# Optimization experiments

Hardware: AMD Instinct MI355X
Metric: run time of the kernel (lower is better)

Reference implementation:

```python
import jax, jax.numpy as jnp
import numpy as np

LAMB = 4.0
TH = -4.0 / LAMB  # threshold from APELoss.__init__
LOSS_WEIGHT = 1.0


def setup_inputs() -> dict:
    key = jax.random.key(0)
    k1, k2 = jax.random.split(key)
    N = 151552  # total anchors
    F = 1024    # foreground anchors (placed first so masks have static shape)
    logits = jax.random.normal(k1, (N,), dtype=jnp.float32)
    targets = jnp.concatenate([jnp.ones((F,), jnp.int32), jnp.zeros((N - F,), jnp.int32)])
    ious = jax.random.uniform(k2, (F,), dtype=jnp.float32)
    return {"logits": logits, "targets": targets, "ious": ious, "num_fg": F}


def reference(logits, targets, ious, num_fg):
    # targets is constructed with all fg (==1) in the first num_fg slots,
    # so logits[targets==1] == logits[:num_fg] (static-shape equivalent).
    fg = logits[:num_fg]          # [F] foreground logits
    bg = logits[num_fg:]          # [B] background logits (targets==0)
    p_min = jnp.min(fg)
    rel_bg = bg >= p_min + TH     # relevant background selection

    # Pairwise fg-vs-bg: [F, B]
    diff_bg = (bg[None, :] - fg[:, None]) * LAMB
    neg_mask = rel_bg[None, :] & (bg[None, :] > fg[:, None] + TH)

    # Pairwise fg-vs-fg: [F, F]
    diff_fg = (fg[None, :] - fg[:, None]) * LAMB
    above = fg[None, :] > fg[:, None] + TH
    pos_mask = (ious[None, :] < ious[:, None]) & above   # lower-IoU fg act as negatives
    tp_mask = (ious[None, :] >= ious[:, None]) & above   # higher/equal-IoU fg are TPs

    # rank = sum sigmoid(FP) + sum sigmoid(TP)  (detached in original)
    fp_sum = (jnp.sum(jax.nn.sigmoid(diff_bg) * neg_mask, axis=1)
              + jnp.sum(jax.nn.sigmoid(diff_fg) * pos_mask, axis=1))
    tp_sum = jnp.sum(jax.nn.sigmoid(diff_fg) * tp_mask, axis=1)
    rank = jax.lax.stop_gradient(fp_sum + tp_sum)

    # BCE(sigmoid(z), 0) = -log(1 - sigmoid(z)) = softplus(z)  (stable form)
    dist = (jnp.sum(jax.nn.softplus(diff_bg) * neg_mask, axis=1)
            + jnp.sum(jax.nn.softplus(diff_fg) * pos_mask, axis=1))

    # Original only appends a loss term when FP_dis is non-empty.
    count = jnp.sum(neg_mask, axis=1) + jnp.sum(pos_mask, axis=1)
    valid = count > 0
    safe_rank = jnp.where(valid, rank, 1.0)
    per = jnp.where(valid, dist * ious / safe_rank, 0.0)
    n_valid = jnp.maximum(jnp.sum(valid), 1)

    return LOSS_WEIGHT * jnp.sum(per) / n_valid.astype(per.dtype) / LAMB
```

## Files before the change

kernel.cpp:

```cpp
#include <hip/hip_runtime.h>
#include <hip/hip_bf16.h>


#define APE_LAMB 4.0f
#define APE_KC   5.770780163555856f
#define APE_LN2  0.6931471805599453f
#define NINF     (-__builtin_inff())

__device__ __forceinline__ float exp2g(float x) { return __builtin_amdgcn_exp2f(x); }
__device__ __forceinline__ float log2g(float x) { return __builtin_amdgcn_logf(x); }
__device__ __forceinline__ float rcpg(float x)  { return __builtin_amdgcn_rcpf(x); }

constexpr int   B_BINS  = 1024;
constexpr int   NB      = 8;
constexpr int   TPB     = 256;
constexpr float BIN_LO  = -5.12f;
constexpr float BIN_DL  = 0.01f;
constexpr float BIN_INV = 100.0f;
constexpr float M1SCALE = 268435456.0f;
constexpr float M1INV   = 3.725290298461914e-09f;
constexpr int   ROWS_E  = 4;
constexpr int   ROWS_B  = 4;

#define ST_AGENT(p, v) __hip_atomic_store((p), (v), __ATOMIC_RELAXED, __HIP_MEMORY_SCOPE_AGENT)
#define LD_AGENT(p)    __hip_atomic_load((p), __ATOMIC_RELAXED, __HIP_MEMORY_SCOPE_AGENT)

__global__ __launch_bounds__(TPB) void ape_phase1(
    const float* __restrict__ logits, const float* __restrict__ ious,
    int F, int M, int chunkH,
    float* __restrict__ gC, float* __restrict__ gM, float* __restrict__ bmaxA,
    float* __restrict__ dist2, float* __restrict__ rank2, float* __restrict__ cnt2,
    int* __restrict__ ctr)
{
    const int tid  = threadIdx.x;
    const int lane = tid & 63, wid = tid >> 6;

    if (blockIdx.x == 0 && tid == 0) *ctr = 0;

    if ((int)blockIdx.x < NB) {
        __shared__ int hc[B_BINS];
        __shared__ int hm[B_BINS];
        for (int b = tid; b < B_BINS; b += TPB) { hc[b] = 0; hm[b] = 0; }
        __syncthreads();

        const float* bg = logits + F;
        const int start = (int)blockIdx.x * chunkH;
        const int end   = min(start + chunkH, M);
        float bmax = NINF;

        for (int j = start + tid * 4; j < end; j += TPB * 4) {
            float v[4];
            if (j + 4 <= end) {
                float4 q = *reinterpret_cast<const float4*>(bg + j);
                v[0] = q.x; v[1] = q.y; v[2] = q.z; v[3] = q.w;
            } else {
#pragma unroll
                for (int k = 0; k < 4; ++k) v[k] = (j + k < end) ? bg[j + k] : NINF;
            }
#pragma unroll
            for (int k = 0; k < 4; ++k) {
                if (j + k >= end) continue;
                float x = v[k];
                bmax = fmaxf(bmax, x);
                int b = (int)((x - BIN_LO) * BIN_INV);
                b = min(max(b, 0), B_BINS - 1);
                float c = fmaf((float)b, BIN_DL, BIN_LO + 0.5f * BIN_DL);
                int q = __float2int_rn((x - c) * M1SCALE);
                atomicAdd(&hc[b], 1);
                atomicAdd(&hm[b], q);
            }
        }
        __syncthreads();
        const int base = (int)blockIdx.x * B_BINS;
        for (int b = tid; b < B_BINS; b += TPB) {
            gC[base + b] = (float)hc[b];
            gM[base + b] = (float)hm[b] * M1INV;
        }
        __shared__ float rm[4];
        for (int off = 32; off > 0; off >>= 1) bmax = fmaxf(bmax, __shfl_down(bmax, off));
        if (lane == 0) rm[wid] = bmax;
        __syncthreads();
        if (tid == 0)
            bmaxA[blockIdx.x] = fmaxf(fmaxf(rm[0], rm[1]), fmaxf(rm[2], rm[3]));
    } else {
        const int i0 = ((int)blockIdx.x - NB) * ROWS_B;
        float fgl[ROWS_B], ioui[ROWS_B];
#pragma unroll
        for (int r = 0; r < ROWS_B; ++r) {
            int i = i0 + r;
            fgl[r]  = (i < F) ? logits[i] * APE_KC : __builtin_inff();
            ioui[r] = (i < F) ? ious[i] : 0.f;
        }
        float dist[ROWS_B], rank[ROWS_B], cnt[ROWS_B];
#pragma unroll
        for (int r = 0; r < ROWS_B; ++r) { dist[r]=0.f; rank[r]=0.f; cnt[r]=0.f; }

        for (int j = tid; j < F; j += TPB) {
            float fjl  = logits[j] * APE_KC;
            float iouj = ious[j];
#pragma unroll
            for (int r = 0; r < ROWS_B; ++r) {
                float dl = fjl - fgl[r];
                bool above = dl > -APE_KC;
                float dm = above ? dl : NINF;
                float u  = exp2g(dm);
                float o  = 1.0f + u;
                float sig = 1.0f - rcpg(o);
                float spl = log2g(o);
                bool pos = iouj < ioui[r];
                rank[r] += sig;
                dist[r] += pos ? spl : 0.f;
                cnt[r]  += (above && pos) ? 1.f : 0.f;
            }
        }
        __shared__ float redf[4][ROWS_B * 3];
#pragma unroll
        for (int r = 0; r < ROWS_B; ++r) {
            float d = dist[r], a = rank[r], c = cnt[r];
            for (int off = 32; off > 0; off >>= 1) {
                d += __shfl_down(d, off);
                a += __shfl_down(a, off);
                c += __shfl_down(c, off);
            }
            if (lane == 0) { redf[wid][r*3+0]=d; redf[wid][r*3+1]=a; redf[wid][r*3+2]=c; }
        }
        __syncthreads();
        if (tid < ROWS_B * 3) {
            float sum = redf[0][tid] + redf[1][tid] + redf[2][tid] + redf[3][tid];
            int r = tid / 3, q = tid % 3;
            int i = i0 + r;
            if (i < F) {
                if      (q == 0) dist2[i] = sum;
                else if (q == 1) rank2[i] = sum;
                else             cnt2[i]  = sum;
            }
        }
    }
}

__global__ __launch_bounds__(TPB) void ape_phase2(
    const float* __restrict__ logits, const float* __restrict__ ious, int F, int EB,
    const float* __restrict__ gC, const float* __restrict__ gM,
    const float* __restrict__ bmaxA,
    const float* __restrict__ dist2, const float* __restrict__ rank2,
    const float* __restrict__ cnt2,
    float* __restrict__ pp, float* __restrict__ pv,
    int* __restrict__ ctr, float* __restrict__ out)
{
    const int tid  = threadIdx.x;
    const int lane = tid & 63, wid = tid >> 6;

    __shared__ float2 h[B_BINS];
    for (int b = tid; b < B_BINS; b += TPB) {
        float c = 0.f, m = 0.f;
#pragma unroll
        for (int s = 0; s < NB; ++s) {
            c += gC[s * B_BINS + b];
            m += gM[s * B_BINS + b];
        }
        h[b] = make_float2(c, m);
    }

    const int i0 = (int)blockIdx.x * ROWS_E;
    float fKC[ROWS_E];
#pragma unroll
    for (int r = 0; r < ROWS_E; ++r) {
        int i = i0 + r;
        fKC[r] = (i < F) ? logits[i] * APE_KC : __builtin_inff();
    }
    __syncthreads();

    float rk[ROWS_E], dt[ROWS_E];
#pragma unroll
    for (int r = 0; r < ROWS_E; ++r) { rk[r] = 0.f; dt[r] = 0.f; }

    for (int it = 0; it < B_BINS; it += TPB) {
        const int b = it + tid;
        float2 cm = h[b];
        float cKC  = fmaf((float)b, BIN_DL * APE_KC, (BIN_LO + 0.5f * BIN_DL) * APE_KC);
        float m1x4 = cm.y * APE_LAMB;
        float m1kc = cm.y * APE_KC;
#pragma unroll
        for (int r = 0; r < ROWS_E; ++r) {
            float dl = cKC - fKC[r];
            float dm = (dl > -APE_KC) ? dl : NINF;
            float u  = exp2g(dm);
            float o  = 1.0f + u;
            float rr = rcpg(o);
            float lg = log2g(o);
            float s  = 1.0f - rr;
            rk[r] = fmaf(cm.x, s,  rk[r]);
            rk[r] = fmaf(m1x4, s * rr, rk[r]);
            dt[r] = fmaf(cm.x, lg, dt[r]);
            dt[r] = fmaf(m1kc, s,  dt[r]);
        }
    }

    __shared__ float red[4][ROWS_E * 2];
#pragma unroll
    for (int r = 0; r < ROWS_E; ++r) {
        float a = rk[r], d = dt[r];
        for (int off = 32; off > 0; off >>= 1) {
            a += __shfl_down(a, off);
            d += __shfl_down(d, off);
        }
        if (lane == 0) { red[wid][r*2+0] = a; red[wid][r*2+1] = d; }
    }
    __syncthreads();

    __shared__ int lastFlag;
    if (tid == 0) {
        float gmax = NINF;
#pragma unroll
        for (int k = 0; k < NB; ++k) gmax = fmaxf(gmax, bmaxA[k]);
        float sper = 0.f, sval = 0.f;
#pragma unroll
        for (int r = 0; r < ROWS_E; ++r) {
            int i = i0 + r;
            if (i < F) {
                float rowRank = red[0][r*2+0] + red[1][r*2+0] + red[2][r*2+0] + red[3][r*2+0];
                float rowDist = red[0][r*2+1] + red[1][r*2+1] + red[2][r*2+1] + red[3][r*2+1];
                float rkv = rowRank + rank2[i];
                float dtv = (rowDist + dist2[i]) * APE_LN2;
                bool valid = (gmax > logits[i] - 1.0f) || (cnt2[i] > 0.f);
                if (valid) {
                    sper += dtv * ious[i] / rkv;
                    sval += 1.f;
                }
            }
        }
        ST_AGENT(&pp[blockIdx.x], sper);
        ST_AGENT(&pv[blockIdx.x], sval);
        asm volatile("s_waitcnt vmcnt(0)" ::: "memory");
        int old = __hip_atomic_fetch_add(ctr, 1, __ATOMIC_RELAXED,
                                         __HIP_MEMORY_SCOPE_AGENT);
        lastFlag = (old == EB - 1) ? 1 : 0;
    }
    __syncthreads();
    if (!lastFlag) return;

    float sp = 0.f, sv = 0.f;
    for (int k = tid; k < EB; k += TPB) {
        sp += LD_AGENT(&pp[k]);
        sv += LD_AGENT(&pv[k]);
    }
    __shared__ float rp[4], rv[4];
    for (int off = 32; off > 0; off >>= 1) {
        sp += __shfl_down(sp, off);
        sv += __shfl_down(sv, off);
    }
    if (lane == 0) { rp[wid] = sp; rv[wid] = sv; }
    __syncthreads();
    if (tid == 0) {
        float p = rp[0] + rp[1] + rp[2] + rp[3];
        float v = rv[0] + rv[1] + rv[2] + rv[3];
        out[0] = p / fmaxf(v, 1.f) / APE_LAMB;
    }
}

extern "C" void kernel_launch(void* const* d_in, const int* in_sizes, int n_in,
                              void* d_out, int out_size, void* d_ws, size_t ws_size,
                              hipStream_t stream) {
    const float* logits = (const float*)d_in[0];
    const float* ious   = (const float*)d_in[2];
    const int N = in_sizes[0];
    const int F = in_sizes[2];
    const int M = N - F;

    const int FB = (F + ROWS_B - 1) / ROWS_B;
    const int EB = (F + ROWS_E - 1) / ROWS_E;

    float* ws    = (float*)d_ws;
    float* gC    = ws;
    float* gM    = gC + NB * B_BINS;
    float* bmaxA = gM + NB * B_BINS;
    float* dist2 = bmaxA + NB;
    float* rank2 = dist2 + F;
    float* cnt2  = rank2 + F;
    float* pp    = cnt2 + F;
    float* pv    = pp + EB;
    int*   ctr   = (int*)(pv + EB);

    int chunkH = ((M + NB - 1) / NB + 3) & ~3;
    if (chunkH < 4) chunkH = 4;

    ape_phase1<<<NB + FB, TPB, 0, stream>>>(logits, ious, F, M, chunkH,
                                            gC, gM, bmaxA, dist2, rank2, cnt2, ctr);
    ape_phase2<<<EB, TPB, 0, stream>>>(logits, ious, F, EB, gC, gM, bmaxA,
                                       dist2, rank2, cnt2, pp, pv, ctr,
                                       (float*)d_out);
}
```

Before: 23.88 us.

## Fuse histogram and evaluation phases into one kernel with spin-wait on counter

Merges the two kernels into a single launch. Eight histogram blocks publish their partial bins and signal an atomic counter, and each evaluation block computes its fg-vs-fg sums before spin-waiting on that counter and then consuming the histogram. This removes one kernel launch and the global round-trip for per-row fg partials. It adds a memset launch and relies on the histogram blocks being scheduled while evaluator blocks spin, which is a deadlock risk if residency is insufficient. The 264 total blocks should fit on the device.

```diff
diff --git a/kernel.cpp b/kernel.cpp
--- a/kernel.cpp
+++ b/kernel.cpp
@@ -19,23 +19,20 @@
 constexpr float BIN_INV = 100.0f;
 constexpr float M1SCALE = 268435456.0f;
 constexpr float M1INV   = 3.725290298461914e-09f;
-constexpr int   ROWS_E  = 4;
-constexpr int   ROWS_B  = 4;
+constexpr int   ROWS    = 4;
 
 #define ST_AGENT(p, v) __hip_atomic_store((p), (v), __ATOMIC_RELAXED, __HIP_MEMORY_SCOPE_AGENT)
 #define LD_AGENT(p)    __hip_atomic_load((p), __ATOMIC_RELAXED, __HIP_MEMORY_SCOPE_AGENT)
 
-__global__ __launch_bounds__(TPB) void ape_phase1(
+__global__ __launch_bounds__(TPB) void ape_fused(
     const float* __restrict__ logits, const float* __restrict__ ious,
-    int F, int M, int chunkH,
+    int F, int M, int chunkH, int NEVAL,
     float* __restrict__ gC, float* __restrict__ gM, float* __restrict__ bmaxA,
-    float* __restrict__ dist2, float* __restrict__ rank2, float* __restrict__ cnt2,
-    int* __restrict__ ctr)
+    float* __restrict__ pp, float* __restrict__ pv,
+    int* __restrict__ ctr, float* __restrict__ out)
 {
     const int tid  = threadIdx.x;
     const int lane = tid & 63, wid = tid >> 6;
-
-    if (blockIdx.x == 0 && tid == 0) *ctr = 0;
 
     if ((int)blockIdx.x < NB) {
         __shared__ int hc[B_BINS];
@@ -73,106 +70,93 @@
         __syncthreads();
         const int base = (int)blockIdx.x * B_BINS;
         for (int b = tid; b < B_BINS; b += TPB) {
-            gC[base + b] = (float)hc[b];
-            gM[base + b] = (float)hm[b] * M1INV;
+            ST_AGENT(&gC[base + b], (float)hc[b]);
+            ST_AGENT(&gM[base + b], (float)hm[b] * M1INV);
         }
         __shared__ float rm[4];
         for (int off = 32; off > 0; off >>= 1) bmax = fmaxf(bmax, __shfl_down(bmax, off));
         if (lane == 0) rm[wid] = bmax;
         __syncthreads();
         if (tid == 0)
-            bmaxA[blockIdx.x] = fmaxf(fmaxf(rm[0], rm[1]), fmaxf(rm[2], rm[3]));
-    } else {
-        const int i0 = ((int)blockIdx.x - NB) * ROWS_B;
-        float fgl[ROWS_B], ioui[ROWS_B];
-#pragma unroll
-        for (int r = 0; r < ROWS_B; ++r) {
-            int i = i0 + r;
-            fgl[r]  = (i < F) ? logits[i] * APE_KC : __builtin_inff();
-            ioui[r] = (i < F) ? ious[i] : 0.f;
-        }
-        float dist[ROWS_B], rank[ROWS_B], cnt[ROWS_B];
-#pragma unroll
-        for (int r = 0; r < ROWS_B; ++r) { dist[r]=0.f; rank[r]=0.f; cnt[r]=0.f; }
-
-        for (int j = tid; j < F; j += TPB) {
-            float fjl  = logits[j] * APE_KC;
-            float iouj = ious[j];
-#pragma unroll
-            for (int r = 0; r < ROWS_B; ++r) {
-                float dl = fjl - fgl[r];
-                bool above = dl > -APE_KC;
-                float dm = above ? dl : NINF;
-                float u  = exp2g(dm);
-                float o  = 1.0f + u;
-                float sig = 1.0f - rcpg(o);
-                float spl = log2g(o);
-                bool pos = iouj < ioui[r];
-                rank[r] += sig;
-                dist[r] += pos ? spl : 0.f;
-                cnt[r]  += (above && pos) ? 1.f : 0.f;
-            }
-        }
-        __shared__ float redf[4][ROWS_B * 3];
-#pragma unroll
-        for (int r = 0; r < ROWS_B; ++r) {
-            float d = dist[r], a = rank[r], c = cnt[r];
-            for (int off = 32; off > 0; off >>= 1) {
-                d += __shfl_down(d, off);
-                a += __shfl_down(a, off);
-                c += __shfl_down(c, off);
-            }
-            if (lane == 0) { redf[wid][r*3+0]=d; redf[wid][r*3+1]=a; redf[wid][r*3+2]=c; }
-        }
-        __syncthreads();
-        if (tid < ROWS_B * 3) {
-            float sum = redf[0][tid] + redf[1][tid] + redf[2][tid] + redf[3][tid];
-            int r = tid / 3, q = tid % 3;
-            int i = i0 + r;
-            if (i < F) {
-                if      (q == 0) dist2[i] = sum;
-                else if (q == 1) rank2[i] = sum;
-                else             cnt2[i]  = sum;
-            }
-        }
-    }
-}
-
-__global__ __launch_bounds__(TPB) void ape_phase2(
-    const float* __restrict__ logits, const float* __restrict__ ious, int F, int EB,
-    const float* __restrict__ gC, const float* __restrict__ gM,
-    const float* __restrict__ bmaxA,
-    const float* __restrict__ dist2, const float* __restrict__ rank2,
-    const float* __restrict__ cnt2,
-    float* __restrict__ pp, float* __restrict__ pv,
-    int* __restrict__ ctr, float* __restrict__ out)
-{
-    const int tid  = threadIdx.x;
-    const int lane = tid & 63, wid = tid >> 6;
+            ST_AGENT(&bmaxA[blockIdx.x],
+                     fmaxf(fmaxf(rm[0], rm[1]), fmaxf(rm[2], rm[3])));
+        asm volatile("s_waitcnt vmcnt(0)" ::: "memory");
+        __syncthreads();
+        if (tid == 0)
+            __hip_atomic_fetch_add(&ctr[0], 1, __ATOMIC_RELAXED,
+                                   __HIP_MEMORY_SCOPE_AGENT);
+        return;
+    }
+
+    const int e  = (int)blockIdx.x - NB;
+    const int i0 = e * ROWS;
+
+    float fKC[ROWS], ioui[ROWS];
+#pragma unroll
+    for (int r = 0; r < ROWS; ++r) {
+        int i = i0 + r;
+        fKC[r]  = (i < F) ? logits[i] * APE_KC : __builtin_inff();
+        ioui[r] = (i < F) ? ious[i] : 0.f;
+    }
+
+    float fdist[ROWS], frank[ROWS], fcnt[ROWS];
+#pragma unroll
+    for (int r = 0; r < ROWS; ++r) { fdist[r]=0.f; frank[r]=0.f; fcnt[r]=0.f; }
+
+    for (int j = tid; j < F; j += TPB) {
+        float fjl  = logits[j] * APE_KC;
+        float iouj = ious[j];
+#pragma unroll
+        for (int r = 0; r < ROWS; ++r) {
+            float dl = fjl - fKC[r];
+            bool above = dl > -APE_KC;
+            float dm = above ? dl : NINF;
+            float u  = exp2g(dm);
+            float o  = 1.0f + u;
+            float sig = 1.0f - rcpg(o);
+            float spl = log2g(o);
+            bool pos = iouj < ioui[r];
+            frank[r] += sig;
+            fdist[r] += pos ? spl : 0.f;
+            fcnt[r]  += (above && pos) ? 1.f : 0.f;
+        }
+    }
+    __shared__ float redf[4][ROWS * 3];
+    __shared__ float fg3[ROWS * 3];
+#pragma unroll
+    for (int r = 0; r < ROWS; ++r) {
+        float a = frank[r], d = fdist[r], c = fcnt[r];
+        for (int off = 32; off > 0; off >>= 1) {
+            a += __shfl_down(a, off);
+            d += __shfl_down(d, off);
+            c += __shfl_down(c, off);
+        }
+        if (lane == 0) { redf[wid][r*3+0]=a; redf[wid][r*3+1]=d; redf[wid][r*3+2]=c; }
+    }
+    __syncthreads();
+    if (tid < ROWS * 3)
+        fg3[tid] = redf[0][tid] + redf[1][tid] + redf[2][tid] + redf[3][tid];
+
+    if (tid == 0) {
+        while (LD_AGENT(&ctr[0]) < NB) __builtin_amdgcn_s_sleep(8);
+    }
+    __syncthreads();
 
     __shared__ float2 h[B_BINS];
     for (int b = tid; b < B_BINS; b += TPB) {
         float c = 0.f, m = 0.f;
 #pragma unroll
         for (int s = 0; s < NB; ++s) {
-            c += gC[s * B_BINS + b];
-            m += gM[s * B_BINS + b];
+            c += LD_AGENT(&gC[s * B_BINS + b]);
+            m += LD_AGENT(&gM[s * B_BINS + b]);
         }
         h[b] = make_float2(c, m);
     }
-
-    const int i0 = (int)blockIdx.x * ROWS_E;
-    float fKC[ROWS_E];
-#pragma unroll
-    for (int r = 0; r < ROWS_E; ++r) {
-        int i = i0 + r;
-        fKC[r] = (i < F) ? logits[i] * APE_KC : __builtin_inff();
-    }
-    __syncthreads();
-
-    float rk[ROWS_E], dt[ROWS_E];
-#pragma unroll
-    for (int r = 0; r < ROWS_E; ++r) { rk[r] = 0.f; dt[r] = 0.f; }
+    __syncthreads();
+
+    float rk[ROWS], dt[ROWS];
+#pragma unroll
+    for (int r = 0; r < ROWS; ++r) { rk[r] = 0.f; dt[r] = 0.f; }
 
     for (int it = 0; it < B_BINS; it += TPB) {
         const int b = it + tid;
@@ -181,7 +165,7 @@
         float m1x4 = cm.y * APE_LAMB;
         float m1kc = cm.y * APE_KC;
 #pragma unroll
-        for (int r = 0; r < ROWS_E; ++r) {
+        for (int r = 0; r < ROWS; ++r) {
             float dl = cKC - fKC[r];
             float dm = (dl > -APE_KC) ? dl : NINF;
             float u  = exp2g(dm);
@@ -196,9 +180,9 @@
         }
     }
 
-    __shared__ float red[4][ROWS_E * 2];
-#pragma unroll
-    for (int r = 0; r < ROWS_E; ++r) {
+    __shared__ float red[4][ROWS * 2];
+#pragma unroll
+    for (int r = 0; r < ROWS; ++r) {
         float a = rk[r], d = dt[r];
         for (int off = 32; off > 0; off >>= 1) {
             a += __shfl_down(a, off);
@@ -212,35 +196,35 @@
     if (tid == 0) {
         float gmax = NINF;
 #pragma unroll
-        for (int k = 0; k < NB; ++k) gmax = fmaxf(gmax, bmaxA[k]);
+        for (int k = 0; k < NB; ++k) gmax = fmaxf(gmax, LD_AGENT(&bmaxA[k]));
         float sper = 0.f, sval = 0.f;
 #pragma unroll
-        for (int r = 0; r < ROWS_E; ++r) {
+        for (int r = 0; r < ROWS; ++r) {
             int i = i0 + r;
             if (i < F) {
                 float rowRank = red[0][r*2+0] + red[1][r*2+0] + red[2][r*2+0] + red[3][r*2+0];
                 float rowDist = red[0][r*2+1] + red[1][r*2+1] + red[2][r*2+1] + red[3][r*2+1];
-                float rkv = rowRank + rank2[i];
-                float dtv = (rowDist + dist2[i]) * APE_LN2;
-                bool valid = (gmax > logits[i] - 1.0f) || (cnt2[i] > 0.f);
+                float rkv = rowRank + fg3[r*3+0];
+                float dtv = (rowDist + fg3[r*3+1]) * APE_LN2;
+                bool valid = (gmax > logits[i] - 1.0f) || (fg3[r*3+2] > 0.f);
                 if (valid) {
                     sper += dtv * ious[i] / rkv;
                     sval += 1.f;
                 }
             }
         }
-        ST_AGENT(&pp[blockIdx.x], sper);
-        ST_AGENT(&pv[blockIdx.x], sval);
+        ST_AGENT(&pp[e], sper);
+        ST_AGENT(&pv[e], sval);
         asm volatile("s_waitcnt vmcnt(0)" ::: "memory");
-        int old = __hip_atomic_fetch_add(ctr, 1, __ATOMIC_RELAXED,
+        int old = __hip_atomic_fetch_add(&ctr[1], 1, __ATOMIC_RELAXED,
                                          __HIP_MEMORY_SCOPE_AGENT);
-        lastFlag = (old == EB - 1) ? 1 : 0;
+        lastFlag = (old == NEVAL - 1) ? 1 : 0;
     }
     __syncthreads();
     if (!lastFlag) return;
 
     float sp = 0.f, sv = 0.f;
-    for (int k = tid; k < EB; k += TPB) {
+    for (int k = tid; k < NEVAL; k += TPB) {
         sp += LD_AGENT(&pp[k]);
         sv += LD_AGENT(&pv[k]);
     }
@@ -254,7 +238,7 @@
     if (tid == 0) {
         float p = rp[0] + rp[1] + rp[2] + rp[3];
         float v = rv[0] + rv[1] + rv[2] + rv[3];
-        out[0] = p / fmaxf(v, 1.f) / APE_LAMB;
+        ST_AGENT(&out[0], p / fmaxf(v, 1.f) / APE_LAMB);
     }
 }
 
@@ -267,26 +251,21 @@
     const int F = in_sizes[2];
     const int M = N - F;
 
-    const int FB = (F + ROWS_B - 1) / ROWS_B;
-    const int EB = (F + ROWS_E - 1) / ROWS_E;
+    const int NEVAL = (F + ROWS - 1) / ROWS;
 
     float* ws    = (float*)d_ws;
     float* gC    = ws;
     float* gM    = gC + NB * B_BINS;
     float* bmaxA = gM + NB * B_BINS;
-    float* dist2 = bmaxA + NB;
-    float* rank2 = dist2 + F;
-    float* cnt2  = rank2 + F;
-    float* pp    = cnt2 + F;
-    float* pv    = pp + EB;
-    int*   ctr   = (int*)(pv + EB);
+    float* pp    = bmaxA + NB;
+    float* pv    = pp + NEVAL;
+    int*   ctr   = (int*)(pv + NEVAL);
 
     int chunkH = ((M + NB - 1) / NB + 3) & ~3;
     if (chunkH < 4) chunkH = 4;
 
-    ape_phase1<<<NB + FB, TPB, 0, stream>>>(logits, ious, F, M, chunkH,
-                                            gC, gM, bmaxA, dist2, rank2, cnt2, ctr);
-    ape_phase2<<<EB, TPB, 0, stream>>>(logits, ious, F, EB, gC, gM, bmaxA,
-                                       dist2, rank2, cnt2, pp, pv, ctr,
-                                       (float*)d_out);
+    hipMemsetAsync(ctr, 0, 2 * sizeof(int), stream);
+    ape_fused<<<NB + NEVAL, TPB, 0, stream>>>(logits, ious, F, M, chunkH, NEVAL,
+                                              gC, gM, bmaxA, pp, pv, ctr,
+                                              (float*)d_out);
 }
```

Measured after the change: 29.35 us. 1.23x slower.
